# Optimization experiments

Measured on AMD Instinct MI355X. Metric: run time of the kernel, lower is better.

Reference implementation:

```python
import jax, jax.numpy as jnp
import numpy as np

N = 200000   # nodes
E = 6400000  # edges
F = 128      # input features
H = 16       # hidden dim (fixed in module)
C = 10       # num classes
B = 512      # graphs in batch


def setup_inputs() -> dict:
    key = jax.random.key(0)
    ks = jax.random.split(key, 9)
    x = jax.random.normal(ks[0], (N, F), dtype=jnp.float32)
    edge_index = jax.random.randint(ks[1], (2, E), 0, N, dtype=jnp.int64)
    batch = jnp.sort(jax.random.randint(ks[2], (N,), 0, B, dtype=jnp.int64))
    W1 = jax.random.normal(ks[3], (F, H), dtype=jnp.float32) * 0.1
    b1 = jnp.zeros((H,), dtype=jnp.float32)
    W2 = jax.random.normal(ks[4], (H, H), dtype=jnp.float32) * 0.1
    b2 = jnp.zeros((H,), dtype=jnp.float32)
    Wfc = jax.random.normal(ks[5], (H, C), dtype=jnp.float32) * 0.1
    bfc = jnp.zeros((C,), dtype=jnp.float32)
    return {"x": x, "edge_index": edge_index, "batch": batch,
            "W1": W1, "b1": b1, "W2": W2, "b2": b2, "Wfc": Wfc, "bfc": bfc}


def reference(x, edge_index, batch, W1, b1, W2, b2, Wfc, bfc):
    row, col = edge_index[0], edge_index[1]  # source -> target
    ones_e = jnp.ones((E,), dtype=x.dtype)
    # GCN symmetric norm with implicit self-loops: deg = 1 + in-degree
    deg = 1.0 + jax.ops.segment_sum(ones_e, col, num_segments=N)
    dis = deg ** -0.5                         # [N]
    norm = dis[row] * dis[col]                # [E], self-loop norm = 1/deg

    def gcn_conv(h, W, b):
        hw = h @ W                             # [N, out]
        msg = norm[:, None] * hw[row]          # [E, out]
        agg = jax.ops.segment_sum(msg, col, num_segments=N)
        agg = agg + hw * (1.0 / deg)[:, None]  # self-loop contribution
        return agg + b

    h = jax.nn.relu(gcn_conv(x, W1, b1))
    h = gcn_conv(h, W2, b2)
    # global mean pool over graphs
    ones_n = jnp.ones((N,), dtype=h.dtype)
    counts = jax.ops.segment_sum(ones_n, batch, num_segments=B)
    sums = jax.ops.segment_sum(h, batch, num_segments=B)
    pooled = sums / jnp.maximum(counts, 1.0)[:, None]  # [B, H]
    return pooled @ Wfc + bfc                           # [B, C]
```

## Files before the change

kernel.cpp:

```cpp
#include <hip/hip_runtime.h>

#define N_ 200000
#define E_ 6400000
#define F_ 128
#define H_ 16
#define C_ 10
#define B_ 512

#define CSH   15
#define NCH   7
#define SBSH  11
#define NSB   98
#define NKEY  (NCH * NSB)
#define NT    256
#define EPT   25000
#define N1    (N_ + 1)
#define STG2  11520
#define AGGB  1563

__global__ __launch_bounds__(1024) void k_count1(const int* __restrict__ row, const int* __restrict__ col,
                                                 int* __restrict__ cnt1) {
    __shared__ int hist[NKEY];
    int tid = threadIdx.x, tile = blockIdx.x;
    for (int i = tid; i < NKEY; i += 1024) hist[i] = 0;
    __syncthreads();
    const int* r = row + (size_t)tile * EPT;
    const int* c = col + (size_t)tile * EPT;
    for (int i = tid; i < EPT; i += 1024) {
        int key = (r[i] >> CSH) * NSB + (c[i] >> SBSH);
        atomicAdd(&hist[key], 1);
    }
    __syncthreads();
    for (int i = tid; i < NKEY; i += 1024) cnt1[(size_t)i * NT + tile] = hist[i];
}

__global__ __launch_bounds__(256) void k_scan_col(int* __restrict__ cnt_mat, int* __restrict__ keyTotal) {
    __shared__ int s[256];
    int k = blockIdx.x, t = threadIdx.x;
    int v[4];
    int seg = 0;
#pragma unroll
    for (int j = 0; j < 4; ++j) {
        int idx = 4 * t + j;
        v[j] = (idx < NT) ? cnt_mat[(size_t)k * NT + idx] : 0;
        seg += v[j];
    }
    s[t] = seg;
    __syncthreads();
    for (int off = 1; off < 256; off <<= 1) {
        int tmp = (t >= off) ? s[t - off] : 0;
        __syncthreads();
        s[t] += tmp;
        __syncthreads();
    }
    if (t == 255) keyTotal[k] = s[255];
    int running = s[t] - seg;
#pragma unroll
    for (int j = 0; j < 4; ++j) {
        int idx = 4 * t + j;
        if (idx < NT) {
            int old = v[j];
            cnt_mat[(size_t)k * NT + idx] = running;
            running += old;
        }
    }
}

__global__ __launch_bounds__(1024) void k_scan_top(const int* __restrict__ keyTotal, int* __restrict__ keyStart, int n) {
    __shared__ int s[1024];
    int t = threadIdx.x;
    int v = (t < n) ? keyTotal[t] : 0;
    s[t] = v;
    __syncthreads();
    for (int off = 1; off < 1024; off <<= 1) {
        int tmp = (t >= off) ? s[t - off] : 0;
        __syncthreads();
        s[t] += tmp;
        __syncthreads();
    }
    if (t < n) keyStart[t] = s[t] - v;
    if (t == n - 1) keyStart[n] = s[t];
}

__global__ __launch_bounds__(1024) void k_part1(const int* __restrict__ row, const int* __restrict__ col,
                                                const int* __restrict__ cnt1, const int* __restrict__ ks1,
                                                unsigned int* __restrict__ edges1) {
    __shared__ int cur[NKEY];
    int tid = threadIdx.x, tile = blockIdx.x;
    for (int i = tid; i < NKEY; i += 1024) cur[i] = cnt1[(size_t)i * NT + tile] + ks1[i];
    __syncthreads();
    const int* r = row + (size_t)tile * EPT;
    const int* c = col + (size_t)tile * EPT;
    for (int i = tid; i < EPT; i += 1024) {
        int src = r[i], dst = c[i];
        int key = (src >> CSH) * NSB + (dst >> SBSH);
        int p = atomicAdd(&cur[key], 1);
        edges1[p] = ((unsigned int)(dst & 2047) << CSH) | (unsigned int)(src & 32767);
    }
}

__global__ __launch_bounds__(256) void k_part2(unsigned int* __restrict__ edges1, const int* __restrict__ ks1,
                                               unsigned short* __restrict__ off16, unsigned int* __restrict__ spill) {
    __shared__ unsigned int stg[STG2];
    __shared__ int cnt[2048];
    __shared__ int aux[256];
    int b = blockIdx.x, tid = threadIdx.x;
    int c = b / NSB, sb = b % NSB;
    int s = ks1[b], e = ks1[b + 1], len = e - s;
    if (sb == NSB - 1 && tid == 0) off16[(size_t)c * N1 + N_] = (unsigned short)len;
    for (int i = tid; i < 2048; i += 256) cnt[i] = 0;
    __syncthreads();
    bool small = (len <= STG2);
    if (small) {
        for (int i = tid; i < len; i += 256) {
            unsigned int w = edges1[s + i];
            stg[i] = w;
            atomicAdd(&cnt[w >> CSH], 1);
        }
    } else {
        for (int i = tid; i < len; i += 256) {
            unsigned int w = edges1[s + i];
            spill[s + i] = w;
            atomicAdd(&cnt[w >> CSH], 1);
        }
    }
    __syncthreads();
    int base = tid * 8;
    int vals[8];
    int run = 0;
#pragma unroll
    for (int j = 0; j < 8; ++j) { vals[j] = cnt[base + j]; run += vals[j]; }
    aux[tid] = run;
    __syncthreads();
    for (int o = 1; o < 256; o <<= 1) {
        int tmp = (tid >= o) ? aux[tid - o] : 0;
        __syncthreads();
        aux[tid] += tmp;
        __syncthreads();
    }
    int acc = aux[tid] - run;
    int nb = (sb << SBSH) + base;
#pragma unroll
    for (int j = 0; j < 8; ++j) {
        int v = vals[j];
        cnt[base + j] = acc;
        int n = nb + j;
        if (n < N_) off16[(size_t)c * N1 + n] = (unsigned short)acc;
        acc += v;
    }
    __syncthreads();
    if (small) {
        for (int i = tid; i < len; i += 256) {
            unsigned int w = stg[i];
            int pos = atomicAdd(&cnt[w >> CSH], 1);
            edges1[s + pos] = ((unsigned int)c << CSH) | (w & 32767u);
        }
    } else {
        for (int i = tid; i < len; i += 256) {
            unsigned int w = spill[s + i];
            int pos = atomicAdd(&cnt[w >> CSH], 1);
            edges1[s + pos] = ((unsigned int)c << CSH) | (w & 32767u);
        }
    }
}

__global__ __launch_bounds__(256) void k_gemm1s(const float* __restrict__ x, const float* __restrict__ W1,
                                                const unsigned short* __restrict__ off16, const int* __restrict__ ks1g,
                                                float* __restrict__ dis, float* __restrict__ P) {
    __shared__ float w[F_ * H_];
    __shared__ int ks[NKEY + 1];
    for (int i = threadIdx.x; i < F_ * H_; i += 256) w[i] = W1[i];
    for (int i = threadIdx.x; i <= NKEY; i += 256) ks[i] = ks1g[i];
    __syncthreads();
    int n = blockIdx.x * 256 + threadIdx.x;
    if (n >= N_) return;
    int sb = n >> SBSH, sb1 = (n + 1) >> SBSH;
    int deg = 0;
#pragma unroll
    for (int c = 0; c < NCH; ++c) {
        int s = ks[c * NSB + sb]  + off16[(size_t)c * N1 + n];
        int e = ks[c * NSB + sb1] + off16[(size_t)c * N1 + n + 1];
        deg += e - s;
    }
    float dn = rsqrtf(1.0f + (float)deg);
    dis[n] = dn;
    float acc[H_];
#pragma unroll
    for (int h = 0; h < H_; ++h) acc[h] = 0.f;
    const float4* xr = reinterpret_cast<const float4*>(x + (size_t)n * F_);
#pragma unroll 4
    for (int k4 = 0; k4 < F_ / 4; ++k4) {
        float4 xv = xr[k4];
        int k = k4 * 4;
#pragma unroll
        for (int h = 0; h < H_; ++h) {
            acc[h] += xv.x * w[(k + 0) * H_ + h] + xv.y * w[(k + 1) * H_ + h]
                    + xv.z * w[(k + 2) * H_ + h] + xv.w * w[(k + 3) * H_ + h];
        }
    }
    float* o = P + (size_t)n * H_;
#pragma unroll
    for (int h = 0; h < H_; h += 4)
        *(float4*)(o + h) = make_float4(acc[h] * dn, acc[h + 1] * dn, acc[h + 2] * dn, acc[h + 3] * dn);
}

__global__ __launch_bounds__(256) void k_gemm2s(const float* __restrict__ hin, const float* __restrict__ W2,
                                                const float* __restrict__ dis, float* __restrict__ P) {
    __shared__ float w[H_ * H_];
    if (threadIdx.x < H_ * H_) w[threadIdx.x] = W2[threadIdx.x];
    __syncthreads();
    int n = blockIdx.x * 256 + threadIdx.x;
    if (n >= N_) return;
    float hv[H_];
    const float4* hr = reinterpret_cast<const float4*>(hin + (size_t)n * H_);
#pragma unroll
    for (int q = 0; q < 4; ++q) {
        float4 v = hr[q];
        hv[q * 4 + 0] = v.x; hv[q * 4 + 1] = v.y; hv[q * 4 + 2] = v.z; hv[q * 4 + 3] = v.w;
    }
    float acc[H_];
#pragma unroll
    for (int h = 0; h < H_; ++h) acc[h] = 0.f;
#pragma unroll
    for (int k = 0; k < H_; ++k)
#pragma unroll
        for (int h = 0; h < H_; ++h) acc[h] += hv[k] * w[k * H_ + h];
    float dn = dis[n];
    float* o = P + (size_t)n * H_;
#pragma unroll
    for (int h = 0; h < H_; h += 4)
        *(float4*)(o + h) = make_float4(acc[h] * dn, acc[h + 1] * dn, acc[h + 2] * dn, acc[h + 3] * dn);
}

template <int RELU>
__global__ __launch_bounds__(256) void k_agg(const float4* __restrict__ P4, const unsigned int* __restrict__ csr,
                                             const unsigned short* __restrict__ off16, const int* __restrict__ ks1g,
                                             const float* __restrict__ dis, const float* __restrict__ bias,
                                             float4* __restrict__ Q4) {
    __shared__ int ks[NKEY + 1];
    for (int i = threadIdx.x; i <= NKEY; i += 256) ks[i] = ks1g[i];
    __syncthreads();
    int g = threadIdx.x >> 2, hq = threadIdx.x & 3;
    int n0 = blockIdx.x * 128 + g * 2;
    if (n0 >= N_) return;
    int sb  = n0 >> SBSH;
    int sbE = (n0 + 2) >> SBSH;
    float4 acc0 = {0,0,0,0}, acc1 = {0,0,0,0};
    const unsigned short* ob = off16 + n0;
    ushort2 o2 = *(const ushort2*)ob;
    unsigned short oE = ob[2];
#pragma unroll
    for (int c = 0; c < NCH; ++c) {
        int bs = ks[c * NSB + sb];
        int be = ks[c * NSB + sbE];
        int s0 = bs + o2.x;
        int s1 = bs + o2.y;
        int e1 = be + oE;
        if (c + 1 < NCH) {
            const unsigned short* obn = off16 + (size_t)(c + 1) * N1 + n0;
            o2 = *(const ushort2*)obn;
            oE = obn[2];
        }
#pragma unroll 4
        for (int p = s0; p < e1; ++p) {
            float4 v = P4[(size_t)csr[p] * 4 + hq];
            float w0 = (p < s1) ? 1.f : 0.f;
            float w1 = 1.f - w0;
            acc0.x += w0 * v.x; acc0.y += w0 * v.y; acc0.z += w0 * v.z; acc0.w += w0 * v.w;
            acc1.x += w1 * v.x; acc1.y += w1 * v.y; acc1.z += w1 * v.z; acc1.w += w1 * v.w;
        }
    }
    float2 d2 = *(const float2*)(dis + n0);
    float4 b4 = ((const float4*)bias)[hq];
#define FINISH(ACC, K, DN)                                            \
    {                                                                 \
        float4 self = P4[(size_t)(n0 + K) * 4 + hq];                  \
        float4 v;                                                     \
        v.x = (DN) * (ACC.x + self.x) + b4.x;                         \
        v.y = (DN) * (ACC.y + self.y) + b4.y;                         \
        v.z = (DN) * (ACC.z + self.z) + b4.z;                         \
        v.w = (DN) * (ACC.w + self.w) + b4.w;                         \
        if (RELU) {                                                   \
            v.x = fmaxf(v.x, 0.f); v.y = fmaxf(v.y, 0.f);             \
            v.z = fmaxf(v.z, 0.f); v.w = fmaxf(v.w, 0.f);             \
        }                                                             \
        Q4[(size_t)(n0 + K) * 4 + hq] = v;                            \
    }
    FINISH(acc0, 0, d2.x)
    FINISH(acc1, 1, d2.y)
#undef FINISH
}

__global__ __launch_bounds__(256) void k_pool_fc(const float* __restrict__ h2, const int* __restrict__ batch,
                                                 const float* __restrict__ Wfc, const float* __restrict__ bfc,
                                                 float* __restrict__ out) {
    int b = blockIdx.x;
    int lo = 0, hi = N_;
    while (lo < hi) { int m = (lo + hi) >> 1; if (batch[m] < b) lo = m + 1; else hi = m; }
    int start = lo;
    lo = start; hi = N_;
    while (lo < hi) { int m = (lo + hi) >> 1; if (batch[m] < b + 1) lo = m + 1; else hi = m; }
    int end = lo;

    int t = threadIdx.x;
    int h = t & 15, q = t >> 4;
    float acc = 0.f;
    for (int n = start + q; n < end; n += 16) acc += h2[(size_t)n * H_ + h];
    acc += __shfl_xor(acc, 16);
    acc += __shfl_xor(acc, 32);

    __shared__ float part[4][H_];
    __shared__ float pooled[H_];
    if ((t & 63) < 16) part[t >> 6][h] = acc;
    __syncthreads();
    if (t < H_) {
        float s2 = part[0][t] + part[1][t] + part[2][t] + part[3][t];
        pooled[t] = s2 / fmaxf((float)(end - start), 1.0f);
    }
    __syncthreads();
    if (t < C_) {
        float o = bfc[t];
#pragma unroll
        for (int hh = 0; hh < H_; ++hh) o += pooled[hh] * Wfc[hh * C_ + t];
        out[b * C_ + t] = o;
    }
}

extern "C" void kernel_launch(void* const* d_in, const int* in_sizes, int n_in,
                              void* d_out, int out_size, void* d_ws, size_t ws_size,
                              hipStream_t stream) {
    const float* x    = (const float*)d_in[0];
    const int*   ei   = (const int*)d_in[1];
    const int*   batch= (const int*)d_in[2];
    const float* W1   = (const float*)d_in[3];
    const float* b1   = (const float*)d_in[4];
    const float* W2   = (const float*)d_in[5];
    const float* b2   = (const float*)d_in[6];
    const float* Wfc  = (const float*)d_in[7];
    const float* bfc  = (const float*)d_in[8];
    float* out = (float*)d_out;

    const int* row = ei;
    const int* col = ei + E_;

    size_t off = 0;
    auto alloc = [&](size_t bytes) -> void* {
        void* p = (char*)d_ws + off;
        off += (bytes + 255) & ~(size_t)255;
        return p;
    };
    char*           U        = (char*)alloc((size_t)NCH * N1 * 2);
    int*            cnt1     = (int*)U;
    unsigned short* off16    = (unsigned short*)U;
    int*            keyTotal = (int*)alloc((size_t)NKEY * 4);
    int*            ks1      = (int*)alloc((size_t)(NKEY + 1) * 4);
    unsigned int*   edges1   = (unsigned int*)alloc((size_t)E_ * 4);
    float*          dis      = (float*)alloc((size_t)N_ * 4);
    float*          P        = (float*)alloc((size_t)N_ * H_ * 4);
    float*          Q        = (float*)alloc((size_t)N_ * H_ * 4);
    unsigned int*   spill    = (unsigned int*)P;
    (void)ws_size; (void)in_sizes; (void)n_in; (void)out_size;

    const int gridN = (N_ + 255) / 256;

    k_count1  <<<NT, 1024, 0, stream>>>(row, col, cnt1);
    k_scan_col<<<NKEY, 256, 0, stream>>>(cnt1, keyTotal);
    k_scan_top<<<1, 1024, 0, stream>>>(keyTotal, ks1, NKEY);
    k_part1   <<<NT, 1024, 0, stream>>>(row, col, cnt1, ks1, edges1);
    k_part2   <<<NKEY, 256, 0, stream>>>(edges1, ks1, off16, spill);

    k_gemm1s<<<gridN, 256, 0, stream>>>(x, W1, off16, ks1, dis, P);
    k_agg<1><<<AGGB, 256, 0, stream>>>((const float4*)P, edges1, off16, ks1, dis, b1, (float4*)Q);
    k_gemm2s<<<gridN, 256, 0, stream>>>(Q, W2, dis, P);
    k_agg<0><<<AGGB, 256, 0, stream>>>((const float4*)P, edges1, off16, ks1, dis, b2, (float4*)Q);

    k_pool_fc<<<B_, 256, 0, stream>>>(Q, batch, Wfc, bfc, out);
}
```

Baseline: 300.7 us.

## Split gemm1 K-dimension across 4 lanes with two nodes per quad

The first-layer projection kernel now assigns four lanes to each pair of nodes. Each lane handles a 32-wide slice of the 128 input features, and the partial sums are combined with cross-lane shuffles. W1 is replicated into four padded shared-memory copies so each lane group reads its own slice without bank conflicts. The aim is to make the x row loads coalesced, keep loads in flight and reduce per-thread register pressure, at the cost of extra shuffle reductions and a larger shared-memory footprint.

```diff
diff --git a/kernel.cpp b/kernel.cpp
--- a/kernel.cpp
+++ b/kernel.cpp
@@ -17,6 +17,8 @@
 #define N1    (N_ + 1)
 #define STG2  11520
 #define AGGB  1563
+#define G1B   1563
+#define WSTR  2052
 
 __global__ __launch_bounds__(1024) void k_count1(const int* __restrict__ row, const int* __restrict__ col,
                                                  int* __restrict__ cnt1) {
@@ -167,41 +169,76 @@
 __global__ __launch_bounds__(256) void k_gemm1s(const float* __restrict__ x, const float* __restrict__ W1,
                                                 const unsigned short* __restrict__ off16, const int* __restrict__ ks1g,
                                                 float* __restrict__ dis, float* __restrict__ P) {
-    __shared__ float w[F_ * H_];
+    __shared__ float wsh[4 * WSTR];
     __shared__ int ks[NKEY + 1];
-    for (int i = threadIdx.x; i < F_ * H_; i += 256) w[i] = W1[i];
+    for (int i = threadIdx.x; i < F_ * H_; i += 256) {
+        float v = W1[i];
+        wsh[i] = v; wsh[WSTR + i] = v; wsh[2 * WSTR + i] = v; wsh[3 * WSTR + i] = v;
+    }
     for (int i = threadIdx.x; i <= NKEY; i += 256) ks[i] = ks1g[i];
     __syncthreads();
-    int n = blockIdx.x * 256 + threadIdx.x;
-    if (n >= N_) return;
-    int sb = n >> SBSH, sb1 = (n + 1) >> SBSH;
-    int deg = 0;
-#pragma unroll
-    for (int c = 0; c < NCH; ++c) {
-        int s = ks[c * NSB + sb]  + off16[(size_t)c * N1 + n];
-        int e = ks[c * NSB + sb1] + off16[(size_t)c * N1 + n + 1];
-        deg += e - s;
-    }
-    float dn = rsqrtf(1.0f + (float)deg);
-    dis[n] = dn;
-    float acc[H_];
-#pragma unroll
-    for (int h = 0; h < H_; ++h) acc[h] = 0.f;
-    const float4* xr = reinterpret_cast<const float4*>(x + (size_t)n * F_);
-#pragma unroll 4
-    for (int k4 = 0; k4 < F_ / 4; ++k4) {
-        float4 xv = xr[k4];
-        int k = k4 * 4;
-#pragma unroll
-        for (int h = 0; h < H_; ++h) {
-            acc[h] += xv.x * w[(k + 0) * H_ + h] + xv.y * w[(k + 1) * H_ + h]
-                    + xv.z * w[(k + 2) * H_ + h] + xv.w * w[(k + 3) * H_ + h];
-        }
-    }
-    float* o = P + (size_t)n * H_;
-#pragma unroll
-    for (int h = 0; h < H_; h += 4)
-        *(float4*)(o + h) = make_float4(acc[h] * dn, acc[h + 1] * dn, acc[h + 2] * dn, acc[h + 3] * dn);
+    int t = blockIdx.x * 256 + threadIdx.x;
+    int p = t >> 2, q = t & 3;
+    int n0 = p * 2;
+    if (n0 >= N_) return;
+    int sb00 = n0 >> SBSH, sb01 = (n0 + 1) >> SBSH, sbE = (n0 + 2) >> SBSH;
+    int deg0 = 0, deg1 = 0;
+    for (int c = q; c < NCH; c += 4) {
+        const unsigned short* ob = off16 + (size_t)c * N1 + n0;
+        ushort2 o2 = *(const ushort2*)ob;
+        unsigned short oE = ob[2];
+        deg0 += (ks[c * NSB + sb01] + o2.y) - (ks[c * NSB + sb00] + o2.x);
+        deg1 += (ks[c * NSB + sbE] + oE) - (ks[c * NSB + sb01] + o2.y);
+    }
+    deg0 += __shfl_xor(deg0, 1); deg0 += __shfl_xor(deg0, 2);
+    deg1 += __shfl_xor(deg1, 1); deg1 += __shfl_xor(deg1, 2);
+    float dn0 = rsqrtf(1.0f + (float)deg0);
+    float dn1 = rsqrtf(1.0f + (float)deg1);
+    if (q == 0) dis[n0] = dn0;
+    if (q == 1) dis[n0 + 1] = dn1;
+    const float4* xr0 = (const float4*)(x + (size_t)n0 * F_) + q * 8;
+    const float4* xr1 = (const float4*)(x + (size_t)(n0 + 1) * F_) + q * 8;
+    const float4* wq = (const float4*)(wsh + q * WSTR + (q << 9));
+    float4 a0q0 = {0,0,0,0}, a0q1 = {0,0,0,0}, a0q2 = {0,0,0,0}, a0q3 = {0,0,0,0};
+    float4 a1q0 = {0,0,0,0}, a1q1 = {0,0,0,0}, a1q2 = {0,0,0,0}, a1q3 = {0,0,0,0};
+#define KSTEP(KL, XS0, XS1)                                                        \
+    {                                                                              \
+        float4 w0 = wq[(KL) * 4 + 0], w1 = wq[(KL) * 4 + 1];                       \
+        float4 w2 = wq[(KL) * 4 + 2], w3 = wq[(KL) * 4 + 3];                       \
+        a0q0.x += (XS0) * w0.x; a0q0.y += (XS0) * w0.y; a0q0.z += (XS0) * w0.z; a0q0.w += (XS0) * w0.w; \
+        a0q1.x += (XS0) * w1.x; a0q1.y += (XS0) * w1.y; a0q1.z += (XS0) * w1.z; a0q1.w += (XS0) * w1.w; \
+        a0q2.x += (XS0) * w2.x; a0q2.y += (XS0) * w2.y; a0q2.z += (XS0) * w2.z; a0q2.w += (XS0) * w2.w; \
+        a0q3.x += (XS0) * w3.x; a0q3.y += (XS0) * w3.y; a0q3.z += (XS0) * w3.z; a0q3.w += (XS0) * w3.w; \
+        a1q0.x += (XS1) * w0.x; a1q0.y += (XS1) * w0.y; a1q0.z += (XS1) * w0.z; a1q0.w += (XS1) * w0.w; \
+        a1q1.x += (XS1) * w1.x; a1q1.y += (XS1) * w1.y; a1q1.z += (XS1) * w1.z; a1q1.w += (XS1) * w1.w; \
+        a1q2.x += (XS1) * w2.x; a1q2.y += (XS1) * w2.y; a1q2.z += (XS1) * w2.z; a1q2.w += (XS1) * w2.w; \
+        a1q3.x += (XS1) * w3.x; a1q3.y += (XS1) * w3.y; a1q3.z += (XS1) * w3.z; a1q3.w += (XS1) * w3.w; \
+    }
+#pragma unroll
+    for (int kk4 = 0; kk4 < 8; ++kk4) {
+        float4 xa = xr0[kk4];
+        float4 xb = xr1[kk4];
+        int klb = kk4 * 4;
+        KSTEP(klb + 0, xa.x, xb.x)
+        KSTEP(klb + 1, xa.y, xb.y)
+        KSTEP(klb + 2, xa.z, xb.z)
+        KSTEP(klb + 3, xa.w, xb.w)
+    }
+#undef KSTEP
+#define RED(F)                                                                     \
+    F.x += __shfl_xor(F.x, 1); F.y += __shfl_xor(F.y, 1); F.z += __shfl_xor(F.z, 1); F.w += __shfl_xor(F.w, 1); \
+    F.x += __shfl_xor(F.x, 2); F.y += __shfl_xor(F.y, 2); F.z += __shfl_xor(F.z, 2); F.w += __shfl_xor(F.w, 2);
+    RED(a0q0) RED(a0q1) RED(a0q2) RED(a0q3)
+    RED(a1q0) RED(a1q1) RED(a1q2) RED(a1q3)
+#undef RED
+    float4 s0 = (q == 0) ? a0q0 : (q == 1) ? a0q1 : (q == 2) ? a0q2 : a0q3;
+    float4 s1 = (q == 0) ? a1q0 : (q == 1) ? a1q1 : (q == 2) ? a1q2 : a1q3;
+    float4* P4 = (float4*)P;
+    float4 o0, o1;
+    o0.x = s0.x * dn0; o0.y = s0.y * dn0; o0.z = s0.z * dn0; o0.w = s0.w * dn0;
+    o1.x = s1.x * dn1; o1.y = s1.y * dn1; o1.z = s1.z * dn1; o1.w = s1.w * dn1;
+    P4[(size_t)n0 * 4 + q] = o0;
+    P4[(size_t)(n0 + 1) * 4 + q] = o1;
 }
 
 __global__ __launch_bounds__(256) void k_gemm2s(const float* __restrict__ hin, const float* __restrict__ W2,
@@ -369,7 +406,7 @@
     k_part1   <<<NT, 1024, 0, stream>>>(row, col, cnt1, ks1, edges1);
     k_part2   <<<NKEY, 256, 0, stream>>>(edges1, ks1, off16, spill);
 
-    k_gemm1s<<<gridN, 256, 0, stream>>>(x, W1, off16, ks1, dis, P);
+    k_gemm1s<<<G1B, 256, 0, stream>>>(x, W1, off16, ks1, dis, P);
     k_agg<1><<<AGGB, 256, 0, stream>>>((const float4*)P, edges1, off16, ks1, dis, b1, (float4*)Q);
     k_gemm2s<<<gridN, 256, 0, stream>>>(Q, W2, dis, P);
     k_agg<0><<<AGGB, 256, 0, stream>>>((const float4*)P, edges1, off16, ks1, dis, b2, (float4*)Q);
```

Measured after the change: 304.2 us. No clear change (+1.2%).
